# Kernel tuning notes

Measured on AMD Instinct MI355X. Metric: run time of the kernel, lower is better.

Reference implementation:

```python
import jax, jax.numpy as jnp
import numpy as np

B, T, D = 8, 1024, 768
N_HEAD = 12
HEAD_DIM = D // N_HEAD


def setup_inputs() -> dict:
    key = jax.random.key(0)
    k1, k2, k3, k4, k5 = jax.random.split(key, 5)
    x = jax.random.normal(k1, (B, T, D), dtype=jnp.float32)
    # c_attn: Linear(D, 3D); c_proj: Linear(D, D). Stored as (in, out) for x @ W.
    s_attn = 1.0 / np.sqrt(D)
    W_attn = jax.random.uniform(k2, (D, 3 * D), dtype=jnp.float32, minval=-s_attn, maxval=s_attn)
    b_attn = jax.random.uniform(k3, (3 * D,), dtype=jnp.float32, minval=-s_attn, maxval=s_attn)
    W_proj = jax.random.uniform(k4, (D, D), dtype=jnp.float32, minval=-s_attn, maxval=s_attn)
    b_proj = jax.random.uniform(k5, (D,), dtype=jnp.float32, minval=-s_attn, maxval=s_attn)
    return {"x": x, "W_attn": W_attn, "b_attn": b_attn, "W_proj": W_proj, "b_proj": b_proj}


def reference(x, W_attn, b_attn, W_proj, b_proj):
    Bs, Ts, Ds = x.shape
    qkv = x @ W_attn + b_attn  # [B, T, 3D]
    Q, K, V = jnp.split(qkv, 3, axis=2)
    # [B, H, T, hd]
    Q = Q.reshape(Bs, Ts, N_HEAD, HEAD_DIM).transpose(0, 2, 1, 3)
    K = K.reshape(Bs, Ts, N_HEAD, HEAD_DIM).transpose(0, 2, 1, 3)
    V = V.reshape(Bs, Ts, N_HEAD, HEAD_DIM).transpose(0, 2, 1, 3)
    scale = HEAD_DIM ** (-0.5)
    scores = jnp.einsum('bhqd,bhkd->bhqk', Q, K) * scale  # [B, H, T, T]
    causal = jnp.tril(jnp.ones((Ts, Ts), dtype=bool))
    scores = jnp.where(causal[None, None, :, :], scores, -jnp.inf)
    probs = jax.nn.softmax(scores, axis=-1)
    attn = jnp.einsum('bhqk,bhkd->bhqd', probs, V)  # [B, H, T, hd]
    attn = attn.transpose(0, 2, 1, 3).reshape(Bs, Ts, Ds)
    return attn @ W_proj + b_proj
```

## Files before the change

### kernel.cpp

```cpp
#include <hip/hip_runtime.h>
#include <hip/hip_bf16.h>

#define B_ 8
#define T_ 1024
#define D_ 768
#define NH 12
#define HD 64

typedef __bf16 bf16x8 __attribute__((ext_vector_type(8)));
typedef __bf16 bf16x4 __attribute__((ext_vector_type(4)));
typedef float f32x4 __attribute__((ext_vector_type(4)));
typedef short s16x4 __attribute__((ext_vector_type(4)));

__device__ __forceinline__ float fast_exp2(float x) {
  return __builtin_amdgcn_exp2f(x);
}

__device__ __forceinline__ f32x4 mfma32(bf16x8 a, bf16x8 b, f32x4 c) {
  return __builtin_amdgcn_mfma_f32_16x16x32_bf16(a, b, c, 0, 0, 0);
}

__device__ __forceinline__ f32x4 mfma16(bf16x4 a, bf16x4 b, f32x4 c) {
  union U { bf16x4 h; s16x4 s; };
  U ua; ua.h = a;
  U ub; ub.h = b;
  return __builtin_amdgcn_mfma_f32_16x16x16bf16_1k(ua.s, ub.s, c, 0, 0, 0);
}

__device__ __forceinline__ void gload_lds16(const void* g, void* l) {
  __builtin_amdgcn_global_load_lds((const __attribute__((address_space(1))) unsigned int*)g,
                                   (__attribute__((address_space(3))) unsigned int*)l, 16, 0, 0);
}

__global__ void prep_kernel(const float* __restrict__ x, __bf16* __restrict__ xb,
                            const float* __restrict__ W_attn, __bf16* __restrict__ WaT,
                            const float* __restrict__ W_proj, __bf16* __restrict__ WpT) {
  int bid = blockIdx.x;
  int tid = threadIdx.x;
  if (bid < 3072) {
    int i = bid * 256 + tid;
    const float4* xf = (const float4*)x;
    float4 a = xf[i * 2], b = xf[i * 2 + 1];
    bf16x8 v;
    v[0] = (__bf16)a.x; v[1] = (__bf16)a.y; v[2] = (__bf16)a.z; v[3] = (__bf16)a.w;
    v[4] = (__bf16)b.x; v[5] = (__bf16)b.y; v[6] = (__bf16)b.z; v[7] = (__bf16)b.w;
    *(bf16x8*)&xb[(size_t)i * 8] = v;
    return;
  }
  __shared__ float tile[32][33];
  const float* W;
  __bf16* WT;
  int K = 768, N, n0, k0;
  if (bid < 4800) {
    int i = bid - 3072;
    W = W_attn; WT = WaT; N = 2304;
    n0 = (i % 72) * 32; k0 = (i / 72) * 32;
  } else {
    int i = bid - 4800;
    W = W_proj; WT = WpT; N = 768;
    n0 = (i % 24) * 32; k0 = (i / 24) * 32;
  }
  int col = tid & 31, r0 = tid >> 5;
#pragma unroll
  for (int p = 0; p < 4; p++) {
    int r = r0 + p * 8;
    tile[r][col] = W[(size_t)(k0 + r) * N + n0 + col];
  }
  __syncthreads();
#pragma unroll
  for (int p = 0; p < 4; p++) {
    int r = r0 + p * 8;
    WT[(size_t)(n0 + r) * K + k0 + col] = (__bf16)tile[col][r];
  }
}

__global__ __launch_bounds__(256) void gemm_qkv(const __bf16* __restrict__ A,
                                                const __bf16* __restrict__ BT,
                                                const float* __restrict__ bias,
                                                __bf16* __restrict__ Cout,
                                                __bf16* __restrict__ VT,
                                                int M, int N, int K, int nbx) {
  __shared__ __align__(16) __bf16 Asm[2][128 * 64];
  __shared__ __align__(16) __bf16 Bsm[2][128 * 64];
  int tid = threadIdx.x;
  int wave = tid >> 6, lane = tid & 63, g = lane >> 4, l15 = lane & 15;
  int wr = wave >> 1, wc = wave & 1;

  int wg = blockIdx.x;
  int cpx = gridDim.x >> 3;
  int wg2 = (wg & 7) * cpx + (wg >> 3);
  int bx = wg2 % nbx, by = wg2 / nbx;
  int m0 = by * 128, n0 = bx * 128;

  int srow = tid >> 3;
  int cc = (tid & 7) ^ ((tid >> 3) & 7);
  const __bf16* Ag = A + (size_t)(m0 + srow) * K + cc * 8;
  const __bf16* Bg = BT + (size_t)(n0 + srow) * K + cc * 8;

  auto stage = [&](int kt, int bf) {
#pragma unroll
    for (int i = 0; i < 4; i++) {
      gload_lds16(Ag + (size_t)(i * 32) * K + kt * 64, &Asm[bf][wave * 512 + i * 2048]);
      gload_lds16(Bg + (size_t)(i * 32) * K + kt * 64, &Bsm[bf][wave * 512 + i * 2048]);
    }
  };

  f32x4 zz = {0.0f, 0.0f, 0.0f, 0.0f};
  f32x4 acc[4][4];
#pragma unroll
  for (int m = 0; m < 4; m++)
#pragma unroll
    for (int n = 0; n < 4; n++) acc[m][n] = zz;

  int nk = K >> 6;
  int swr = l15 & 7;

  stage(0, 0);
  __syncthreads();

  int cur = 0;
  for (int kt = 0; kt < nk; kt++) {
    if (kt + 1 < nk) stage(kt + 1, cur ^ 1);
#pragma unroll
    for (int ks = 0; ks < 2; ks++) {
      bf16x8 af[4], bfr[4];
#pragma unroll
      for (int m = 0; m < 4; m++) {
        int row = wr * 64 + m * 16 + l15;
        af[m] = *(const bf16x8*)&Asm[cur][row * 64 + ((ks * 4 + g) ^ swr) * 8];
      }
#pragma unroll
      for (int n = 0; n < 4; n++) {
        int row = wc * 64 + n * 16 + l15;
        bfr[n] = *(const bf16x8*)&Bsm[cur][row * 64 + ((ks * 4 + g) ^ swr) * 8];
      }
#pragma unroll
      for (int m = 0; m < 4; m++)
#pragma unroll
        for (int n = 0; n < 4; n++)
          acc[m][n] = __builtin_amdgcn_mfma_f32_16x16x32_bf16(af[m], bfr[n], acc[m][n], 0, 0, 0);
    }
    __syncthreads();
    cur ^= 1;
  }
#pragma unroll
  for (int n = 0; n < 4; n++) {
    int gcol = n0 + wc * 64 + n * 16 + l15;
    float bv = bias[gcol];
#pragma unroll
    for (int m = 0; m < 4; m++) {
      int grow0 = m0 + wr * 64 + m * 16 + g * 4;
      float v0 = acc[m][n][0] + bv, v1 = acc[m][n][1] + bv;
      float v2 = acc[m][n][2] + bv, v3 = acc[m][n][3] + bv;
      if (gcol < 2 * D_) {
        Cout[(size_t)(grow0 + 0) * N + gcol] = (__bf16)v0;
        Cout[(size_t)(grow0 + 1) * N + gcol] = (__bf16)v1;
        Cout[(size_t)(grow0 + 2) * N + gcol] = (__bf16)v2;
        Cout[(size_t)(grow0 + 3) * N + gcol] = (__bf16)v3;
      } else {
        int hh = (gcol - 2 * D_) >> 6, dd = (gcol - 2 * D_) & 63;
        int bb = grow0 >> 10, tt = grow0 & 1023;
        bf16x4 sv = {(__bf16)v0, (__bf16)v1, (__bf16)v2, (__bf16)v3};
        *(bf16x4*)&VT[((size_t)(bb * NH + hh) * HD + dd) * T_ + tt] = sv;
      }
    }
  }
}

__global__ __launch_bounds__(256) void gemm_proj(const __bf16* __restrict__ A,
                                                 const __bf16* __restrict__ BT,
                                                 const float* __restrict__ bias,
                                                 float* __restrict__ Cout,
                                                 int M, int N, int K, int nbx) {
  __shared__ __align__(16) __bf16 Asm[2][128 * 64];
  __shared__ __align__(16) __bf16 Bsm[2][64 * 64];
  int tid = threadIdx.x;
  int wave = tid >> 6, lane = tid & 63, g = lane >> 4, l15 = lane & 15;

  int wg = blockIdx.x;
  int cpx = gridDim.x >> 3;
  int wg2 = (wg & 7) * cpx + (wg >> 3);
  int bx = wg2 % nbx, by = wg2 / nbx;
  int m0 = by * 128, n0 = bx * 64;

  int srow = tid >> 3;
  int cc = (tid & 7) ^ ((tid >> 3) & 7);
  const __bf16* Ag = A + (size_t)(m0 + srow) * K + cc * 8;
  const __bf16* Bg = BT + (size_t)(n0 + srow) * K + cc * 8;

  auto stage = [&](int kt, int bf) {
#pragma unroll
    for (int i = 0; i < 4; i++)
      gload_lds16(Ag + (size_t)(i * 32) * K + kt * 64, &Asm[bf][wave * 512 + i * 2048]);
#pragma unroll
    for (int i = 0; i < 2; i++)
      gload_lds16(Bg + (size_t)(i * 32) * K + kt * 64, &Bsm[bf][wave * 512 + i * 2048]);
  };

  f32x4 zz = {0.0f, 0.0f, 0.0f, 0.0f};
  f32x4 acc[2][4];
#pragma unroll
  for (int m = 0; m < 2; m++)
#pragma unroll
    for (int n = 0; n < 4; n++) acc[m][n] = zz;

  int nk = K >> 6;
  int swr = l15 & 7;

  stage(0, 0);
  __syncthreads();

  int cur = 0;
  for (int kt = 0; kt < nk; kt++) {
    if (kt + 1 < nk) stage(kt + 1, cur ^ 1);
#pragma unroll
    for (int ks = 0; ks < 2; ks++) {
      bf16x8 af[2], bfr[4];
#pragma unroll
      for (int m = 0; m < 2; m++) {
        int row = wave * 32 + m * 16 + l15;
        af[m] = *(const bf16x8*)&Asm[cur][row * 64 + ((ks * 4 + g) ^ swr) * 8];
      }
#pragma unroll
      for (int n = 0; n < 4; n++) {
        int row = n * 16 + l15;
        bfr[n] = *(const bf16x8*)&Bsm[cur][row * 64 + ((ks * 4 + g) ^ swr) * 8];
      }
#pragma unroll
      for (int m = 0; m < 2; m++)
#pragma unroll
        for (int n = 0; n < 4; n++)
          acc[m][n] = __builtin_amdgcn_mfma_f32_16x16x32_bf16(af[m], bfr[n], acc[m][n], 0, 0, 0);
    }
    __syncthreads();
    cur ^= 1;
  }
#pragma unroll
  for (int n = 0; n < 4; n++) {
    int gcol = n0 + n * 16 + l15;
    float bv = bias[gcol];
#pragma unroll
    for (int m = 0; m < 2; m++) {
      int grow0 = m0 + wave * 32 + m * 16 + g * 4;
#pragma unroll
      for (int r = 0; r < 4; r++)
        Cout[(size_t)(grow0 + r) * N + gcol] = acc[m][n][r] + bv;
    }
  }
}

#define SCL 0.1803368801111204f

__global__ __launch_bounds__(256, 4) void attn_kernel(const __bf16* __restrict__ qkv,
                                                      const __bf16* __restrict__ VT,
                                                      __bf16* __restrict__ attn_out) {
  __shared__ __align__(16) __bf16 sm[2][2][4096];
  int tid = threadIdx.x;
  int wave = tid >> 6, lane = tid & 63, g = lane >> 4, l15 = lane & 15;
  int bh = blockIdx.x;
  int b = bh / NH, h = bh % NH;
  int qb = 15 - blockIdx.y;
  int q0w = qb * 64 + wave * 16;
  int nkt = qb + 1;
  int s0 = (bh + qb) % nkt;

  int kr = tid >> 3, cc = (tid & 7) ^ ((tid >> 3) & 7);
  const __bf16* Kst = qkv + (size_t)(b * T_ + kr) * (3 * D_) + D_ + h * HD + cc * 8;
  const __bf16* Vst = VT + ((size_t)bh * HD + kr) * T_ + cc * 8;
  __bf16* ldsK0 = &sm[0][0][wave * 512];
  __bf16* ldsV0 = &sm[0][1][wave * 512];
  __bf16* ldsK1 = &sm[1][0][wave * 512];
  __bf16* ldsV1 = &sm[1][1][wave * 512];

  auto stage = [&](int t, int bf) {
    size_t ko = (size_t)(t * 64) * (3 * D_);
    int vo = t * 64;
    __bf16* lk = bf ? ldsK1 : ldsK0;
    __bf16* lv = bf ? ldsV1 : ldsV0;
    gload_lds16(Kst + ko, lk);
    gload_lds16(Kst + ko + (size_t)32 * (3 * D_), lk + 2048);
    gload_lds16(Vst + vo, lv);
    gload_lds16(Vst + vo + 32 * T_, lv + 2048);
  };

  const __bf16* Qp = qkv + (size_t)(b * T_ + q0w + l15) * (3 * D_) + h * HD;
  bf16x8 qlo = *(const bf16x8*)(Qp + g * 8);
  bf16x8 qhi = *(const bf16x8*)(Qp + 32 + g * 8);

  f32x4 zz = {0.0f, 0.0f, 0.0f, 0.0f};
  f32x4 o0 = zz, o1 = zz, o2 = zz, o3 = zz;
  float m = -1e30f, l = 0.0f;
  int sw = l15 & 7;
  int clo = (g ^ sw) * 8;
  int chi = ((4 + g) ^ sw) * 8;

  stage(s0, 0);
  __syncthreads();

  int cur = 0;
  for (int i = 0; i < nkt; i++) {
    int kt = s0 + i;
    if (kt >= nkt) kt -= nkt;
    if (i + 1 < nkt) stage(kt + 1 == nkt ? 0 : kt + 1, cur ^ 1);

    const __bf16* Kb = &sm[cur][0][0];
    f32x4 s[4];
    __builtin_amdgcn_s_setprio(1);
#pragma unroll
    for (int kg = 0; kg < 4; kg++) {
      int rb = (kg * 16 + l15) * 64;
      bf16x8 kf = *(const bf16x8*)(Kb + rb + clo);
      bf16x8 kh = *(const bf16x8*)(Kb + rb + chi);
      s[kg] = mfma32(kf, qlo, zz);
      s[kg] = mfma32(kh, qhi, s[kg]);
    }
    __builtin_amdgcn_s_setprio(0);

    float v[16];
#pragma unroll
    for (int kg = 0; kg < 4; kg++)
#pragma unroll
      for (int r = 0; r < 4; r++) v[kg * 4 + r] = s[kg][r] * SCL;
    if (kt == qb) {
      int thr = wave * 16 + l15;
#pragma unroll
      for (int kg = 0; kg < 4; kg++)
#pragma unroll
        for (int r = 0; r < 4; r++)
          if (kg * 16 + g * 4 + r > thr) v[kg * 4 + r] = -1e30f;
    }
    float m0a = fmaxf(fmaxf(v[0], v[1]), fmaxf(v[2], v[3]));
    float m1a = fmaxf(fmaxf(v[4], v[5]), fmaxf(v[6], v[7]));
    float m2a = fmaxf(fmaxf(v[8], v[9]), fmaxf(v[10], v[11]));
    float m3a = fmaxf(fmaxf(v[12], v[13]), fmaxf(v[14], v[15]));
    float mx = fmaxf(fmaxf(m0a, m1a), fmaxf(m2a, m3a));
    mx = fmaxf(mx, __shfl_xor(mx, 16));
    mx = fmaxf(mx, __shfl_xor(mx, 32));
    if (!__all(mx <= m + 8.0f)) {
      float mnew = fmaxf(m, mx);
      float corr = fast_exp2(m - mnew);
      o0 *= corr; o1 *= corr; o2 *= corr; o3 *= corr;
      l *= corr;
      m = mnew;
    }
    float p[16], sum = 0.0f;
#pragma unroll
    for (int i2 = 0; i2 < 16; i2++) { p[i2] = fast_exp2(v[i2] - m); sum += p[i2]; }
    sum += __shfl_xor(sum, 16);
    sum += __shfl_xor(sum, 32);
    l += sum;
    bf16x4 pk[4];
#pragma unroll
    for (int kg = 0; kg < 4; kg++) {
      pk[kg][0] = (__bf16)p[kg * 4 + 0];
      pk[kg][1] = (__bf16)p[kg * 4 + 1];
      pk[kg][2] = (__bf16)p[kg * 4 + 2];
      pk[kg][3] = (__bf16)p[kg * 4 + 3];
    }

    const __bf16* Vb = &sm[cur][1][0];
    int vhalf = (g & 1) * 4;
    int vc = g >> 1;
    __builtin_amdgcn_s_setprio(1);
#pragma unroll
    for (int dq = 0; dq < 4; dq++) {
      int drow = (dq * 16 + l15) * 64;
#pragma unroll
      for (int ks = 0; ks < 4; ks++) {
        bf16x4 vf = *(const bf16x4*)(Vb + drow + ((ks * 2 + vc) ^ sw) * 8 + vhalf);
        f32x4* op = (dq == 0) ? &o0 : (dq == 1) ? &o1 : (dq == 2) ? &o2 : &o3;
        *op = mfma16(vf, pk[ks], *op);
      }
    }
    __builtin_amdgcn_s_setprio(0);

    __syncthreads();
    cur ^= 1;
  }

  float invl = 1.0f / l;
  __bf16* outp = attn_out + (size_t)(b * T_ + q0w + l15) * D_ + h * HD + g * 4;
  bf16x4 t0 = {(__bf16)(o0[0] * invl), (__bf16)(o0[1] * invl), (__bf16)(o0[2] * invl), (__bf16)(o0[3] * invl)};
  bf16x4 t1 = {(__bf16)(o1[0] * invl), (__bf16)(o1[1] * invl), (__bf16)(o1[2] * invl), (__bf16)(o1[3] * invl)};
  bf16x4 t2 = {(__bf16)(o2[0] * invl), (__bf16)(o2[1] * invl), (__bf16)(o2[2] * invl), (__bf16)(o2[3] * invl)};
  bf16x4 t3 = {(__bf16)(o3[0] * invl), (__bf16)(o3[1] * invl), (__bf16)(o3[2] * invl), (__bf16)(o3[3] * invl)};
  *(bf16x4*)(outp) = t0;
  *(bf16x4*)(outp + 16) = t1;
  *(bf16x4*)(outp + 32) = t2;
  *(bf16x4*)(outp + 48) = t3;
}

extern "C" void kernel_launch(void* const* d_in, const int* in_sizes, int n_in,
                              void* d_out, int out_size, void* d_ws, size_t ws_size,
                              hipStream_t stream) {
  (void)in_sizes; (void)n_in; (void)out_size; (void)ws_size;
  const float* x = (const float*)d_in[0];
  const float* W_attn = (const float*)d_in[1];
  const float* b_attn = (const float*)d_in[2];
  const float* W_proj = (const float*)d_in[3];
  const float* b_proj = (const float*)d_in[4];

  char* ws = (char*)d_ws;
  __bf16* xb  = (__bf16*)(ws + 0);
  __bf16* WaT = (__bf16*)(ws + 12582912);
  __bf16* WpT = (__bf16*)(ws + 16121856);
  __bf16* qkv = (__bf16*)(ws + 17301504);
  __bf16* VTb = (__bf16*)(ws + 55050240);
  __bf16* att = (__bf16*)(ws + 67633152);

  prep_kernel<<<dim3(5376), 256, 0, stream>>>(x, xb, W_attn, WaT, W_proj, WpT);
  gemm_qkv<<<dim3(1152), 256, 0, stream>>>(xb, WaT, b_attn, qkv, VTb, 8192, 2304, 768, 18);
  attn_kernel<<<dim3(96, 16), 256, 0, stream>>>(qkv, VTb, att);
  gemm_proj<<<dim3(768), 256, 0, stream>>>(att, WpT, b_proj, (float*)d_out, 8192, 768, 768, 12);
}
```

Measured before the change: 111.8 us.

## Process two query blocks per attention workgroup to reuse staged K/V tiles

Each attention workgroup now handles 128 query rows (two 64-row halves) instead of 64, so every K/V tile staged into shared memory feeds two sets of QK and PV MFMAs. This halves K/V global-to-LDS traffic and per-tile barrier overhead relative to compute. The grid shrinks from 96x16 to 96x8 blocks, and launch bounds drop to 3 blocks per CU to make room for the doubled accumulators. The cost is lower occupancy, fewer blocks for load balancing across the causal triangle, and more register pressure.

```diff
diff --git a/kernel.cpp b/kernel.cpp
--- a/kernel.cpp
+++ b/kernel.cpp
@@ -251,7 +251,7 @@
 
 #define SCL 0.1803368801111204f
 
-__global__ __launch_bounds__(256, 4) void attn_kernel(const __bf16* __restrict__ qkv,
+__global__ __launch_bounds__(256, 3) void attn_kernel(const __bf16* __restrict__ qkv,
                                                       const __bf16* __restrict__ VT,
                                                       __bf16* __restrict__ attn_out) {
   __shared__ __align__(16) __bf16 sm[2][2][4096];
@@ -259,9 +259,10 @@
   int wave = tid >> 6, lane = tid & 63, g = lane >> 4, l15 = lane & 15;
   int bh = blockIdx.x;
   int b = bh / NH, h = bh % NH;
-  int qb = 15 - blockIdx.y;
-  int q0w = qb * 64 + wave * 16;
-  int nkt = qb + 1;
+  int qb = 7 - blockIdx.y;
+  int q0a = qb * 128 + wave * 16;
+  int q0b = q0a + 64;
+  int nkt = 2 * qb + 2;
   int s0 = (bh + qb) % nkt;
 
   int kr = tid >> 3, cc = (tid & 7) ^ ((tid >> 3) & 7);
@@ -283,27 +284,27 @@
     gload_lds16(Vst + vo + 32 * T_, lv + 2048);
   };
 
-  const __bf16* Qp = qkv + (size_t)(b * T_ + q0w + l15) * (3 * D_) + h * HD;
-  bf16x8 qlo = *(const bf16x8*)(Qp + g * 8);
-  bf16x8 qhi = *(const bf16x8*)(Qp + 32 + g * 8);
+  const __bf16* Qpa = qkv + (size_t)(b * T_ + q0a + l15) * (3 * D_) + h * HD;
+  const __bf16* Qpb = Qpa + (size_t)64 * (3 * D_);
+  bf16x8 qa_lo = *(const bf16x8*)(Qpa + g * 8);
+  bf16x8 qa_hi = *(const bf16x8*)(Qpa + 32 + g * 8);
+  bf16x8 qb_lo = *(const bf16x8*)(Qpb + g * 8);
+  bf16x8 qb_hi = *(const bf16x8*)(Qpb + 32 + g * 8);
 
   f32x4 zz = {0.0f, 0.0f, 0.0f, 0.0f};
-  f32x4 o0 = zz, o1 = zz, o2 = zz, o3 = zz;
-  float m = -1e30f, l = 0.0f;
+  f32x4 o_a[4], o_b[4];
+#pragma unroll
+  for (int dq = 0; dq < 4; dq++) { o_a[dq] = zz; o_b[dq] = zz; }
+  float m_a = -1e30f, l_a = 0.0f, m_b = -1e30f, l_b = 0.0f;
   int sw = l15 & 7;
   int clo = (g ^ sw) * 8;
   int chi = ((4 + g) ^ sw) * 8;
-
-  stage(s0, 0);
-  __syncthreads();
-
-  int cur = 0;
-  for (int i = 0; i < nkt; i++) {
-    int kt = s0 + i;
-    if (kt >= nkt) kt -= nkt;
-    if (i + 1 < nkt) stage(kt + 1 == nkt ? 0 : kt + 1, cur ^ 1);
-
-    const __bf16* Kb = &sm[cur][0][0];
+  int vhalf = (g & 1) * 4;
+  int vc = g >> 1;
+  int thr = wave * 16 + l15;
+
+  auto tile_body = [&](int masked, const __bf16* Kb, const __bf16* Vb,
+                       bf16x8 qlo, bf16x8 qhi, float& m, float& l, f32x4* o) {
     f32x4 s[4];
     __builtin_amdgcn_s_setprio(1);
 #pragma unroll
@@ -315,14 +316,12 @@
       s[kg] = mfma32(kh, qhi, s[kg]);
     }
     __builtin_amdgcn_s_setprio(0);
-
     float v[16];
 #pragma unroll
     for (int kg = 0; kg < 4; kg++)
 #pragma unroll
       for (int r = 0; r < 4; r++) v[kg * 4 + r] = s[kg][r] * SCL;
-    if (kt == qb) {
-      int thr = wave * 16 + l15;
+    if (masked) {
 #pragma unroll
       for (int kg = 0; kg < 4; kg++)
 #pragma unroll
@@ -339,7 +338,8 @@
     if (!__all(mx <= m + 8.0f)) {
       float mnew = fmaxf(m, mx);
       float corr = fast_exp2(m - mnew);
-      o0 *= corr; o1 *= corr; o2 *= corr; o3 *= corr;
+#pragma unroll
+      for (int dq = 0; dq < 4; dq++) o[dq] *= corr;
       l *= corr;
       m = mnew;
     }
@@ -357,10 +357,6 @@
       pk[kg][2] = (__bf16)p[kg * 4 + 2];
       pk[kg][3] = (__bf16)p[kg * 4 + 3];
     }
-
-    const __bf16* Vb = &sm[cur][1][0];
-    int vhalf = (g & 1) * 4;
-    int vc = g >> 1;
     __builtin_amdgcn_s_setprio(1);
 #pragma unroll
     for (int dq = 0; dq < 4; dq++) {
@@ -368,26 +364,43 @@
 #pragma unroll
       for (int ks = 0; ks < 4; ks++) {
         bf16x4 vf = *(const bf16x4*)(Vb + drow + ((ks * 2 + vc) ^ sw) * 8 + vhalf);
-        f32x4* op = (dq == 0) ? &o0 : (dq == 1) ? &o1 : (dq == 2) ? &o2 : &o3;
-        *op = mfma16(vf, pk[ks], *op);
+        o[dq] = mfma16(vf, pk[ks], o[dq]);
       }
     }
     __builtin_amdgcn_s_setprio(0);
+  };
+
+  stage(s0, 0);
+  __syncthreads();
+
+  int cur = 0;
+  for (int i = 0; i < nkt; i++) {
+    int kt = s0 + i;
+    if (kt >= nkt) kt -= nkt;
+    if (i + 1 < nkt) stage(kt + 1 == nkt ? 0 : kt + 1, cur ^ 1);
+
+    const __bf16* Kb = &sm[cur][0][0];
+    const __bf16* Vb = &sm[cur][1][0];
+    if (kt != nkt - 1)
+      tile_body(kt == nkt - 2, Kb, Vb, qa_lo, qa_hi, m_a, l_a, o_a);
+    tile_body(kt == nkt - 1, Kb, Vb, qb_lo, qb_hi, m_b, l_b, o_b);
 
     __syncthreads();
     cur ^= 1;
   }
 
-  float invl = 1.0f / l;
-  __bf16* outp = attn_out + (size_t)(b * T_ + q0w + l15) * D_ + h * HD + g * 4;
-  bf16x4 t0 = {(__bf16)(o0[0] * invl), (__bf16)(o0[1] * invl), (__bf16)(o0[2] * invl), (__bf16)(o0[3] * invl)};
-  bf16x4 t1 = {(__bf16)(o1[0] * invl), (__bf16)(o1[1] * invl), (__bf16)(o1[2] * invl), (__bf16)(o1[3] * invl)};
-  bf16x4 t2 = {(__bf16)(o2[0] * invl), (__bf16)(o2[1] * invl), (__bf16)(o2[2] * invl), (__bf16)(o2[3] * invl)};
-  bf16x4 t3 = {(__bf16)(o3[0] * invl), (__bf16)(o3[1] * invl), (__bf16)(o3[2] * invl), (__bf16)(o3[3] * invl)};
-  *(bf16x4*)(outp) = t0;
-  *(bf16x4*)(outp + 16) = t1;
-  *(bf16x4*)(outp + 32) = t2;
-  *(bf16x4*)(outp + 48) = t3;
+  float invla = 1.0f / l_a, invlb = 1.0f / l_b;
+  __bf16* outA = attn_out + (size_t)(b * T_ + q0a + l15) * D_ + h * HD + g * 4;
+  __bf16* outB = outA + (size_t)64 * D_;
+#pragma unroll
+  for (int dq = 0; dq < 4; dq++) {
+    bf16x4 sa = {(__bf16)(o_a[dq][0] * invla), (__bf16)(o_a[dq][1] * invla),
+                 (__bf16)(o_a[dq][2] * invla), (__bf16)(o_a[dq][3] * invla)};
+    bf16x4 sb = {(__bf16)(o_b[dq][0] * invlb), (__bf16)(o_b[dq][1] * invlb),
+                 (__bf16)(o_b[dq][2] * invlb), (__bf16)(o_b[dq][3] * invlb)};
+    *(bf16x4*)(outA + dq * 16) = sa;
+    *(bf16x4*)(outB + dq * 16) = sb;
+  }
 }
 
 extern "C" void kernel_launch(void* const* d_in, const int* in_sizes, int n_in,
@@ -410,6 +423,6 @@
 
   prep_kernel<<<dim3(5376), 256, 0, stream>>>(x, xb, W_attn, WaT, W_proj, WpT);
   gemm_qkv<<<dim3(1152), 256, 0, stream>>>(xb, WaT, b_attn, qkv, VTb, 8192, 2304, 768, 18);
-  attn_kernel<<<dim3(96, 16), 256, 0, stream>>>(qkv, VTb, att);
+  attn_kernel<<<dim3(96, 8), 256, 0, stream>>>(qkv, VTb, att);
   gemm_proj<<<dim3(768), 256, 0, stream>>>(att, WpT, b_proj, (float*)d_out, 8192, 768, 768, 12);
 }
```

New measurement: 116.2 us. 1.04x slower.
